# Optimization experiments

Measured on AMD Instinct MI355X. Metric: run time of the kernel, lower is better.

Reference implementation:

```python
import jax, jax.numpy as jnp
import numpy as np

H_DIM = 768
NUM_HEADS = 12
HEAD_DIM = H_DIM // NUM_HEADS
ROPE_BASE = 10000.0


def rope_cos_sin(seq_len, dim):
    inv_freq = 1.0 / (ROPE_BASE ** (jnp.arange(0, dim, 2, dtype=jnp.float32) / dim))
    t = jnp.arange(seq_len, dtype=jnp.float32)
    freqs = jnp.outer(t, inv_freq)              # [seq, dim/2]
    emb = jnp.concatenate([freqs, freqs], axis=-1)  # [seq, dim]
    return jnp.cos(emb), jnp.sin(emb)


def rotate_half(x):
    x1, x2 = jnp.split(x, 2, axis=-1)
    return jnp.concatenate([-x2, x1], axis=-1)


def setup_inputs() -> dict:
    key = jax.random.key(0)
    ks = jax.random.split(key, 9)
    s = 1.0 / np.sqrt(H_DIM)
    inp = {
        'x': jax.random.normal(ks[0], (2, 8, 1024, H_DIM), dtype=jnp.float32),
        'Wq': jax.random.normal(ks[1], (H_DIM, H_DIM), dtype=jnp.float32) * s,
        'bq': jnp.zeros((H_DIM,), dtype=jnp.float32),
        'Wk': jax.random.normal(ks[2], (H_DIM, H_DIM), dtype=jnp.float32) * s,
        'bk': jnp.zeros((H_DIM,), dtype=jnp.float32),
        'Wv': jax.random.normal(ks[3], (H_DIM, H_DIM), dtype=jnp.float32) * s,
        'bv': jnp.zeros((H_DIM,), dtype=jnp.float32),
        'Wo': jax.random.normal(ks[4], (H_DIM, H_DIM), dtype=jnp.float32) * s,
        'bo': jnp.zeros((H_DIM,), dtype=jnp.float32),
        'mask': jnp.ones((2, 8, 1, 1, 1024), dtype=jnp.int32),
    }
    return inp


def reference(x, Wq, bq, Wk, bk, Wv, bv, Wo, bo, mask):
    b, r, s, d = x.shape
    H, D = NUM_HEADS, HEAD_DIM

    def proj(W, bvec):
        # [b,r,s,d] -> [b,r,H,s,D]
        y = x @ W + bvec
        return y.reshape(b, r, s, H, D).transpose(0, 1, 3, 2, 4)

    q = proj(Wq, bq)
    k = proj(Wk, bk)
    v = proj(Wv, bv)

    cos, sin = rope_cos_sin(s, D)   # [s, D]
    cos = cos[None, None, None]     # broadcast over b,r,H
    sin = sin[None, None, None]
    q = q * cos + rotate_half(q) * sin
    k = k * cos + rotate_half(k) * sin

    scores = jnp.einsum('brhqd,brhkd->brhqk', q, k) / jnp.sqrt(jnp.float32(D))
    scores = jnp.where(mask == 0, -jnp.inf, scores)
    probs = jax.nn.softmax(scores, axis=-1)  # dropout is identity in eval
    out = jnp.einsum('brhqk,brhkd->brhqd', probs, v)
    out = out.transpose(0, 1, 3, 2, 4).reshape(b, r, s, d)
    return out @ Wo + bo
```

## Files before the change

kernel.cpp:

```cpp
#include <hip/hip_runtime.h>


#define M_TOT 16384
#define DM    768
#define NH    12
#define HD    64
#define SEQ   1024

typedef __attribute__((ext_vector_type(8))) __bf16 bf16x8;
typedef __attribute__((ext_vector_type(4))) __bf16 bf16x4;
typedef __attribute__((ext_vector_type(4))) short s16x4;
typedef __attribute__((ext_vector_type(4))) float  f32x4;

static __device__ __forceinline__ unsigned short f2b(float f) {
  unsigned u = __builtin_bit_cast(unsigned, f);
  u += 0x7FFFu + ((u >> 16) & 1u);
  return (unsigned short)(u >> 16);
}
static __device__ __forceinline__ float b2f(unsigned short s) {
  unsigned u = ((unsigned)s) << 16;
  return __builtin_bit_cast(float, u);
}
static __device__ __forceinline__ unsigned cvt_pk_bf16(float lo, float hi) {
  unsigned d;
  asm("v_cvt_pk_bf16_f32 %0, %1, %2" : "=v"(d) : "v"(lo), "v"(hi));
  return d;
}

static __device__ __forceinline__ f32x4 mfma16(uint2 a, uint2 b, f32x4 c) {
#if __has_builtin(__builtin_amdgcn_mfma_f32_16x16x16_bf16)
  union U { uint2 u; bf16x4 v; } A, B;
  A.u = a; B.u = b;
  return __builtin_amdgcn_mfma_f32_16x16x16_bf16(A.v, B.v, c, 0, 0, 0);
#else
  union U { uint2 u; s16x4 v; } A, B;
  A.u = a; B.u = b;
  return __builtin_amdgcn_mfma_f32_16x16x16bf16_1k(A.v, B.v, c, 0, 0, 0);
#endif
}

static __device__ __forceinline__ void gl_lds16(const void* g, void* l) {
  __builtin_amdgcn_global_load_lds(
      (const __attribute__((address_space(1))) unsigned*)g,
      (__attribute__((address_space(3))) unsigned*)l, 16, 0, 0);
}

static __device__ __forceinline__ int swz_src(int c) {
  return ((c >> 3) << 6) + (((c & 7) ^ ((c >> 3) & 7)) << 3);
}
static __device__ __forceinline__ int swz_rd(int row, int col16) {
  return (row << 6) + ((col16 ^ (row & 7)) << 3);
}

__global__ void cvt_x(const float* __restrict__ x, unsigned short* __restrict__ xb) {
  const int n4 = M_TOT * DM / 4;
  for (int i = blockIdx.x * blockDim.x + threadIdx.x; i < n4; i += gridDim.x * blockDim.x) {
    float4 v = ((const float4*)x)[i];
    ushort4 o;
    o.x = f2b(v.x); o.y = f2b(v.y); o.z = f2b(v.z); o.w = f2b(v.w);
    ((ushort4*)xb)[i] = o;
  }
}

__global__ void prep_w(const float* __restrict__ Wq, const float* __restrict__ Wk,
                       const float* __restrict__ Wv, const float* __restrict__ Wo,
                       unsigned short* __restrict__ Wt) {
  __shared__ float T[64][65];
  const int wsel = blockIdx.z;
  const float* W = wsel == 0 ? Wq : wsel == 1 ? Wk : wsel == 2 ? Wv : Wo;
  const int k0 = blockIdx.x * 64, n0 = blockIdx.y * 64;
  const int t = threadIdx.x;
#pragma unroll
  for (int p = 0; p < 16; ++p) {
    int e = p * 256 + t, r = e >> 6, c = e & 63;
    T[r][c] = W[(size_t)(k0 + r) * DM + n0 + c];
  }
  __syncthreads();
  unsigned short* dst = Wt + (size_t)wsel * DM * DM;
#pragma unroll
  for (int p = 0; p < 16; ++p) {
    int e = p * 256 + t, r = e >> 6, c = e & 63;
    dst[(size_t)(n0 + r) * DM + k0 + c] = f2b(T[c][r]);
  }
}

__global__ void rope_tab(float* __restrict__ cosT, float* __restrict__ sinT) {
  int i = blockIdx.x * blockDim.x + threadIdx.x;
  int s = i >> 5, j = i & 31;
  float inv = powf(10000.0f, -(float)j * (1.0f / 32.0f));
  float ang = (float)s * inv;
  cosT[i] = cosf(ang);
  sinT[i] = sinf(ang);
}

__global__ void bias_cat(const float* __restrict__ bq, const float* __restrict__ bk,
                         const float* __restrict__ bv, float* __restrict__ bcat) {
  int i = blockIdx.x * 256 + threadIdx.x;
  if (i < 3 * DM)
    bcat[i] = i < DM ? bq[i] : (i < 2 * DM ? bk[i - DM] : bv[i - 2 * DM]);
}

static __device__ __forceinline__ void gemm_core(const unsigned short* __restrict__ A,
                                                 const unsigned short* __restrict__ Bt,
                                                 int m0, int n0, f32x4 acc[4][4],
                                                 char* smem) {
  unsigned short* As = (unsigned short*)smem;
  unsigned short* Bs = As + 128 * 64;
  const int tid = threadIdx.x, lane = tid & 63, w = tid >> 6;
  const int wr = w >> 1, wc = w & 1;
  const int lr = lane & 15, g4 = lane >> 4;

#pragma unroll
  for (int i = 0; i < 4; ++i)
#pragma unroll
    for (int j = 0; j < 4; ++j) acc[i][j] = (f32x4){0.f, 0.f, 0.f, 0.f};

  for (int kt = 0; kt < DM / 64; ++kt) {
    const int k0 = kt * 64;
#pragma unroll
    for (int p = 0; p < 4; ++p) {
      int cb = p * 256 + w * 64;
      int c = cb + lane;
      gl_lds16(A + (size_t)(m0 + (c >> 3)) * DM + k0 + (c & 7) * 8, (char*)As + cb * 16);
      gl_lds16(Bt + (size_t)(n0 + (c >> 3)) * DM + k0 + (c & 7) * 8, (char*)Bs + cb * 16);
    }
    __syncthreads();
#pragma unroll
    for (int kk = 0; kk < 2; ++kk) {
      const int ko = kk * 32 + g4 * 8;
      bf16x8 a[4], b[4];
#pragma unroll
      for (int i = 0; i < 4; ++i) a[i] = *(const bf16x8*)&As[(wr * 64 + i * 16 + lr) * 64 + ko];
#pragma unroll
      for (int j = 0; j < 4; ++j) b[j] = *(const bf16x8*)&Bs[(wc * 64 + j * 16 + lr) * 64 + ko];
#pragma unroll
      for (int i = 0; i < 4; ++i)
#pragma unroll
        for (int j = 0; j < 4; ++j)
          acc[i][j] = __builtin_amdgcn_mfma_f32_16x16x32_bf16(a[i], b[j], acc[i][j], 0, 0, 0);
    }
    __syncthreads();
  }
}

__global__ __launch_bounds__(256, 4) void gemm_qkv(
    const unsigned short* __restrict__ xb, const unsigned short* __restrict__ Wt,
    const float* __restrict__ bcat, const float* __restrict__ cosT,
    const float* __restrict__ sinT, unsigned short* __restrict__ Qh,
    unsigned short* __restrict__ Kh, unsigned short* __restrict__ Vt) {
  __shared__ alignas(16) char smem[32768];
  const int m0 = blockIdx.x * 128, n0 = blockIdx.y * 128;
  f32x4 acc[4][4];
  gemm_core(xb, Wt, m0, n0, acc, smem);

  const int tid = threadIdx.x, lane = tid & 63, w = tid >> 6;
  const int wr = w >> 1, wc = w & 1;
  const int lr = lane & 15, g4 = lane >> 4;
  const int zone = blockIdx.y / 6;
  const int wcol0 = n0 - zone * DM + wc * 64;
  const int h = wcol0 >> 6;
  const int br = m0 >> 10;
  const int s_base = (m0 & 1023) + wr * 64;

  if (zone == 2) {
    unsigned short* dstb = Vt + ((size_t)(br * NH + h) * HD) * SEQ;
#pragma unroll
    for (int j = 0; j < 4; ++j) {
      const int d = j * 16 + lr;
      const float bv = bcat[n0 + wc * 64 + d];
#pragma unroll
      for (int i = 0; i < 4; ++i) {
        const int s0 = s_base + i * 16 + g4 * 4;
        ushort4 st;
        st.x = f2b(acc[i][j][0] + bv);
        st.y = f2b(acc[i][j][1] + bv);
        st.z = f2b(acc[i][j][2] + bv);
        st.w = f2b(acc[i][j][3] + bv);
        *(ushort4*)&dstb[(size_t)d * SEQ + s0] = st;
      }
    }
  } else {
    const float sc = zone == 0 ? 0.125f * 1.44269504f : 1.0f;
    unsigned short* dstb = (zone ? Kh : Qh) + ((size_t)(br * NH + h) * SEQ) * HD;
    char* Wb = smem + (size_t)w * 8192;
    const int s_q = s_base + lane;
    const int bcol = n0 + wc * 64;

#pragma unroll
    for (int hh = 0; hh < 2; ++hh) {
#pragma unroll
      for (int jj = 0; jj < 2; ++jj) {
        const int jp = hh + jj * 2;
        const float bv = bcat[bcol + jp * 16 + lr];
        const int dslot = jj * 16 + lr;
        const int sub = (dslot & 3) * 4;
        const int ch = dslot >> 2;
#pragma unroll
        for (int i = 0; i < 4; ++i) {
#pragma unroll
          for (int r = 0; r < 4; ++r) {
            const int s_loc = i * 16 + g4 * 4 + r;
            *(float*)(Wb + s_loc * 128 + ((ch ^ (s_loc & 7)) << 4) + sub) =
                (acc[i][jp][r] + bv) * sc;
          }
        }
      }
      unsigned short* drow = dstb + (size_t)s_q * HD + hh * 16;
      const char* Rb = Wb + lane * 128;
      const int lx = lane & 7;
#pragma unroll
      for (int c = 0; c < 4; ++c) {
        f32x4 va = *(const f32x4*)(Rb + ((c ^ lx) << 4));
        f32x4 vb = *(const f32x4*)(Rb + (((c + 4) ^ lx) << 4));
        float4 c4 = *(const float4*)&cosT[s_q * 32 + hh * 16 + c * 4];
        float4 s4 = *(const float4*)&sinT[s_q * 32 + hh * 16 + c * 4];
        uint2 oa, ob;
        oa.x = cvt_pk_bf16(va[0] * c4.x - vb[0] * s4.x, va[1] * c4.y - vb[1] * s4.y);
        oa.y = cvt_pk_bf16(va[2] * c4.z - vb[2] * s4.z, va[3] * c4.w - vb[3] * s4.w);
        ob.x = cvt_pk_bf16(vb[0] * c4.x + va[0] * s4.x, vb[1] * c4.y + va[1] * s4.y);
        ob.y = cvt_pk_bf16(vb[2] * c4.z + va[2] * s4.z, vb[3] * c4.w + va[3] * s4.w);
        *(uint2*)(drow + c * 4)      = oa;
        *(uint2*)(drow + 32 + c * 4) = ob;
      }
    }
  }
}

__global__ __launch_bounds__(256, 4) void gemm_o(const unsigned short* __restrict__ attnb,
                                                 const unsigned short* __restrict__ WtO,
                                                 const float* __restrict__ bo,
                                                 float* __restrict__ out) {
  __shared__ alignas(16) char smem[32768];
  const int m0 = blockIdx.x * 128, n0 = blockIdx.y * 128;
  f32x4 acc[4][4];
  gemm_core(attnb, WtO, m0, n0, acc, smem);
  const int tid = threadIdx.x, lane = tid & 63, w = tid >> 6;
  const int wr = w >> 1, wc = w & 1;
  const int lr = lane & 15, g4 = lane >> 4;
#pragma unroll
  for (int j = 0; j < 4; ++j) {
    const int col = n0 + wc * 64 + j * 16 + lr;
    const float bv = bo[col];
#pragma unroll
    for (int i = 0; i < 4; ++i) {
      const int rowb = m0 + wr * 64 + i * 16 + g4 * 4;
#pragma unroll
      for (int r = 0; r < 4; ++r)
        out[(size_t)(rowb + r) * DM + col] = acc[i][j][r] + bv;
    }
  }
}

__global__ __launch_bounds__(256) void attn_fwd(const unsigned short* __restrict__ Qh,
                                                const unsigned short* __restrict__ Kh,
                                                const unsigned short* __restrict__ Vt,
                                                const int* __restrict__ mask,
                                                unsigned short* __restrict__ attnb) {
  __shared__ unsigned short Ks[64 * 64];
  __shared__ unsigned short Vs[64 * 64];
  __shared__ float Msf[SEQ];
  const int qt = blockIdx.x, brh = blockIdx.y;
  const int br = brh / NH, h = brh - br * NH;
  const int tid = threadIdx.x, lane = tid & 63, w = tid >> 6;
  const int lr = lane & 15, g4 = lane >> 4;

  {
    int4 mi = *(const int4*)&mask[(size_t)br * SEQ + tid * 4];
    float4 mf;
    mf.x = mi.x ? 0.f : -3e38f;
    mf.y = mi.y ? 0.f : -3e38f;
    mf.z = mi.z ? 0.f : -3e38f;
    mf.w = mi.w ? 0.f : -3e38f;
    *(float4*)&Msf[tid * 4] = mf;
  }

  const unsigned short* Qg = Qh + ((size_t)brh * SEQ + qt * 64 + w * 16 + lr) * HD;
  bf16x8 qa[2];
  qa[0] = *(const bf16x8*)(Qg + g4 * 8);
  qa[1] = *(const bf16x8*)(Qg + 32 + g4 * 8);

  f32x4 o[4];
#pragma unroll
  for (int j = 0; j < 4; ++j) o[j] = (f32x4){0.f, 0.f, 0.f, 0.f};
  float m = -INFINITY;
  float lpA = 0.f, lpB = 0.f;

  const unsigned short* Kg = Kh + (size_t)brh * SEQ * HD;
  const unsigned short* Vg = Vt + (size_t)brh * HD * SEQ;

  for (int kb = 0; kb < SEQ / 64; ++kb) {
#pragma unroll
    for (int p = 0; p < 2; ++p) {
      int cb = p * 256 + w * 64;
      int c = cb + lane;
      gl_lds16(Kg + (size_t)kb * 64 * HD + swz_src(c), (char*)Ks + cb * 16);
      gl_lds16(Vg + (size_t)(c >> 3) * SEQ + kb * 64 + (((c & 7) ^ ((c >> 3) & 7)) << 3),
               (char*)Vs + cb * 16);
    }
    __syncthreads();

    f32x4 s4[4];
#pragma unroll
    for (int j = 0; j < 4; ++j) s4[j] = (f32x4){0.f, 0.f, 0.f, 0.f};
    __builtin_amdgcn_s_setprio(1);
#pragma unroll
    for (int kk = 0; kk < 2; ++kk) {
#pragma unroll
      for (int j = 0; j < 4; ++j) {
        bf16x8 kf = *(const bf16x8*)&Ks[swz_rd(j * 16 + lr, kk * 4 + g4)];
        s4[j] = __builtin_amdgcn_mfma_f32_16x16x32_bf16(kf, qa[kk], s4[j], 0, 0, 0);
      }
    }
    __builtin_amdgcn_s_setprio(0);

    float sv[4][4];
#pragma unroll
    for (int j = 0; j < 4; ++j) {
      float4 mq = *(const float4*)&Msf[kb * 64 + j * 16 + g4 * 4];
      sv[j][0] = s4[j][0] + mq.x;
      sv[j][1] = s4[j][1] + mq.y;
      sv[j][2] = s4[j][2] + mq.z;
      sv[j][3] = s4[j][3] + mq.w;
    }

    float mx = sv[0][0];
#pragma unroll
    for (int j = 0; j < 4; ++j)
#pragma unroll
      for (int r = 0; r < 4; ++r) mx = fmaxf(mx, sv[j][r]);
    mx = fmaxf(mx, __shfl_xor(mx, 16));
    mx = fmaxf(mx, __shfl_xor(mx, 32));
    if (!__all(mx <= m + 8.0f)) {
      float mnew = fmaxf(m, mx);
      float sc = exp2f(m - mnew);
      lpA *= sc; lpB *= sc;
#pragma unroll
      for (int j = 0; j < 4; ++j)
#pragma unroll
        for (int r = 0; r < 4; ++r) o[j][r] *= sc;
      m = mnew;
    }

    uint2 wb[4];
#pragma unroll
    for (int j = 0; j < 4; ++j) {
      float p0 = exp2f(sv[j][0] - m), p1 = exp2f(sv[j][1] - m);
      float p2 = exp2f(sv[j][2] - m), p3 = exp2f(sv[j][3] - m);
      if (j & 1) lpB += (p0 + p1) + (p2 + p3);
      else       lpA += (p0 + p1) + (p2 + p3);
      wb[j].x = cvt_pk_bf16(p0, p1);
      wb[j].y = cvt_pk_bf16(p2, p3);
    }

    __builtin_amdgcn_s_setprio(1);
#pragma unroll
    for (int jj = 0; jj < 4; ++jj) {
      const int row = jj * 16 + lr;
#pragma unroll
      for (int j = 0; j < 4; ++j) {
        const int c8 = j * 4 + g4;
        uint2 av = *(const uint2*)&Vs[(row << 6) + ((((c8 >> 1) ^ (lr & 7))) << 3) +
                                      ((c8 & 1) << 2)];
        o[jj] = mfma16(av, wb[j], o[jj]);
      }
    }
    __builtin_amdgcn_s_setprio(0);
    __syncthreads();
  }

  float lp = lpA + lpB;
  float l = lp + __shfl_xor(lp, 16);
  l += __shfl_xor(l, 32);
  float inv = l > 0.f ? 1.0f / l : 0.f;
  unsigned short* dst =
      attnb + ((size_t)(br * SEQ + qt * 64 + w * 16 + lr)) * DM + h * HD;
#pragma unroll
  for (int j = 0; j < 4; ++j) {
    ushort4 st;
    st.x = f2b(o[j][0] * inv);
    st.y = f2b(o[j][1] * inv);
    st.z = f2b(o[j][2] * inv);
    st.w = f2b(o[j][3] * inv);
    *(ushort4*)&dst[j * 16 + g4 * 4] = st;
  }
}

extern "C" void kernel_launch(void* const* d_in, const int* in_sizes, int n_in,
                              void* d_out, int out_size, void* d_ws, size_t ws_size,
                              hipStream_t stream) {
  const float* x  = (const float*)d_in[0];
  const float* Wq = (const float*)d_in[1];
  const float* bq = (const float*)d_in[2];
  const float* Wk = (const float*)d_in[3];
  const float* bk = (const float*)d_in[4];
  const float* Wv = (const float*)d_in[5];
  const float* bv = (const float*)d_in[6];
  const float* Wo = (const float*)d_in[7];
  const float* bo = (const float*)d_in[8];
  const int* mask = (const int*)d_in[9];
  float* out = (float*)d_out;

  const size_t OFF_XB   = 0;
  const size_t OFF_WT   = 25165824;
  const size_t OFF_COS  = 29884416;
  const size_t OFF_SIN  = 30015488;
  const size_t OFF_BC   = 30146560;
  const size_t OFF_ATT  = 30158848;
  const size_t OFF_QH   = 55324672;
  const size_t OFF_KH   = 80490496;
  const size_t OFF_VT   = 105656320;
  const size_t REQUIRED = 130822144;
  if (ws_size < REQUIRED) return;

  char* w = (char*)d_ws;
  unsigned short* xb   = (unsigned short*)(w + OFF_XB);
  unsigned short* Wt   = (unsigned short*)(w + OFF_WT);
  float* cosT          = (float*)(w + OFF_COS);
  float* sinT          = (float*)(w + OFF_SIN);
  float* bcat          = (float*)(w + OFF_BC);
  unsigned short* attnb = (unsigned short*)(w + OFF_ATT);
  unsigned short* Qh   = (unsigned short*)(w + OFF_QH);
  unsigned short* Kh   = (unsigned short*)(w + OFF_KH);
  unsigned short* Vt   = (unsigned short*)(w + OFF_VT);

  cvt_x<<<2048, 256, 0, stream>>>(x, xb);
  prep_w<<<dim3(12, 12, 4), 256, 0, stream>>>(Wq, Wk, Wv, Wo, Wt);
  rope_tab<<<128, 256, 0, stream>>>(cosT, sinT);
  bias_cat<<<9, 256, 0, stream>>>(bq, bk, bv, bcat);
  gemm_qkv<<<dim3(128, 18), 256, 0, stream>>>(xb, Wt, bcat, cosT, sinT, Qh, Kh, Vt);
  attn_fwd<<<dim3(16, 192), 256, 0, stream>>>(Qh, Kh, Vt, mask, attnb);
  gemm_o<<<dim3(128, 6), 256, 0, stream>>>(attnb, Wt + (size_t)3 * DM * DM, bo, out);
}
```

Before: 268.0 us.

## Double-buffer K/V tiles in attention and skip mask add when all keys live

The attention kernel now keeps two LDS buffers for K and V and issues the async global-to-LDS loads for the next key block before computing on the current one, dropping one barrier per iteration. It also checks once per block whether the whole mask row is nonzero and, if so, skips the per-tile mask loads and adds. The row max is computed with a three-input max tree. The cost is double the K/V LDS footprint, which may lower occupancy. The loop also relies on the end-of-iteration barrier to cover the in-flight async loads, so correctness depends on the compiler inserting a vmcnt wait before that barrier.

```diff
diff --git a/kernel.cpp b/kernel.cpp
--- a/kernel.cpp
+++ b/kernel.cpp
@@ -26,6 +26,7 @@
   asm("v_cvt_pk_bf16_f32 %0, %1, %2" : "=v"(d) : "v"(lo), "v"(hi));
   return d;
 }
+#define MAX3(a, b, c) fmaxf(fmaxf((a), (b)), (c))
 
 static __device__ __forceinline__ f32x4 mfma16(uint2 a, uint2 b, f32x4 c) {
 #if __has_builtin(__builtin_amdgcn_mfma_f32_16x16x16_bf16)
@@ -256,16 +257,20 @@
                                                 const unsigned short* __restrict__ Vt,
                                                 const int* __restrict__ mask,
                                                 unsigned short* __restrict__ attnb) {
-  __shared__ unsigned short Ks[64 * 64];
-  __shared__ unsigned short Vs[64 * 64];
+  __shared__ unsigned short Ks[2][64 * 64];
+  __shared__ unsigned short Vs[2][64 * 64];
   __shared__ float Msf[SEQ];
   const int qt = blockIdx.x, brh = blockIdx.y;
   const int br = brh / NH, h = brh - br * NH;
   const int tid = threadIdx.x, lane = tid & 63, w = tid >> 6;
   const int lr = lane & 15, g4 = lane >> 4;
 
-  {
-    int4 mi = *(const int4*)&mask[(size_t)br * SEQ + tid * 4];
+  const unsigned short* Kg = Kh + (size_t)brh * SEQ * HD;
+  const unsigned short* Vg = Vt + (size_t)brh * HD * SEQ;
+
+  int4 mi = *(const int4*)&mask[(size_t)br * SEQ + tid * 4];
+  const int allLive = __syncthreads_and(mi.x && mi.y && mi.z && mi.w);
+  if (!allLive) {
     float4 mf;
     mf.x = mi.x ? 0.f : -3e38f;
     mf.y = mi.y ? 0.f : -3e38f;
@@ -274,6 +279,15 @@
     *(float4*)&Msf[tid * 4] = mf;
   }
 
+#pragma unroll
+  for (int p = 0; p < 2; ++p) {
+    int cb = p * 256 + w * 64;
+    int c = cb + lane;
+    gl_lds16(Kg + swz_src(c), (char*)Ks[0] + cb * 16);
+    gl_lds16(Vg + (size_t)(c >> 3) * SEQ + (((c & 7) ^ ((c >> 3) & 7)) << 3),
+             (char*)Vs[0] + cb * 16);
+  }
+
   const unsigned short* Qg = Qh + ((size_t)brh * SEQ + qt * 64 + w * 16 + lr) * HD;
   bf16x8 qa[2];
   qa[0] = *(const bf16x8*)(Qg + g4 * 8);
@@ -285,19 +299,25 @@
   float m = -INFINITY;
   float lpA = 0.f, lpB = 0.f;
 
-  const unsigned short* Kg = Kh + (size_t)brh * SEQ * HD;
-  const unsigned short* Vg = Vt + (size_t)brh * HD * SEQ;
+  __syncthreads();
+
+  unsigned short* KsC = Ks[0];
+  unsigned short* VsC = Vs[0];
+  unsigned short* KsN = Ks[1];
+  unsigned short* VsN = Vs[1];
 
   for (int kb = 0; kb < SEQ / 64; ++kb) {
-#pragma unroll
-    for (int p = 0; p < 2; ++p) {
-      int cb = p * 256 + w * 64;
-      int c = cb + lane;
-      gl_lds16(Kg + (size_t)kb * 64 * HD + swz_src(c), (char*)Ks + cb * 16);
-      gl_lds16(Vg + (size_t)(c >> 3) * SEQ + kb * 64 + (((c & 7) ^ ((c >> 3) & 7)) << 3),
-               (char*)Vs + cb * 16);
-    }
-    __syncthreads();
+    if (kb + 1 < SEQ / 64) {
+#pragma unroll
+      for (int p = 0; p < 2; ++p) {
+        int cb = p * 256 + w * 64;
+        int c = cb + lane;
+        gl_lds16(Kg + (size_t)(kb + 1) * 64 * HD + swz_src(c), (char*)KsN + cb * 16);
+        gl_lds16(Vg + (size_t)(c >> 3) * SEQ + (kb + 1) * 64 +
+                     (((c & 7) ^ ((c >> 3) & 7)) << 3),
+                 (char*)VsN + cb * 16);
+      }
+    }
 
     f32x4 s4[4];
 #pragma unroll
@@ -307,27 +327,35 @@
     for (int kk = 0; kk < 2; ++kk) {
 #pragma unroll
       for (int j = 0; j < 4; ++j) {
-        bf16x8 kf = *(const bf16x8*)&Ks[swz_rd(j * 16 + lr, kk * 4 + g4)];
+        bf16x8 kf = *(const bf16x8*)&KsC[swz_rd(j * 16 + lr, kk * 4 + g4)];
         s4[j] = __builtin_amdgcn_mfma_f32_16x16x32_bf16(kf, qa[kk], s4[j], 0, 0, 0);
       }
     }
     __builtin_amdgcn_s_setprio(0);
 
     float sv[4][4];
-#pragma unroll
-    for (int j = 0; j < 4; ++j) {
-      float4 mq = *(const float4*)&Msf[kb * 64 + j * 16 + g4 * 4];
-      sv[j][0] = s4[j][0] + mq.x;
-      sv[j][1] = s4[j][1] + mq.y;
-      sv[j][2] = s4[j][2] + mq.z;
-      sv[j][3] = s4[j][3] + mq.w;
-    }
-
-    float mx = sv[0][0];
-#pragma unroll
-    for (int j = 0; j < 4; ++j)
-#pragma unroll
-      for (int r = 0; r < 4; ++r) mx = fmaxf(mx, sv[j][r]);
+    if (allLive) {
+#pragma unroll
+      for (int j = 0; j < 4; ++j)
+#pragma unroll
+        for (int r = 0; r < 4; ++r) sv[j][r] = s4[j][r];
+    } else {
+#pragma unroll
+      for (int j = 0; j < 4; ++j) {
+        float4 mq = *(const float4*)&Msf[kb * 64 + j * 16 + g4 * 4];
+        sv[j][0] = s4[j][0] + mq.x;
+        sv[j][1] = s4[j][1] + mq.y;
+        sv[j][2] = s4[j][2] + mq.z;
+        sv[j][3] = s4[j][3] + mq.w;
+      }
+    }
+
+    float t0 = MAX3(sv[0][0], sv[0][1], sv[0][2]);
+    float t1 = MAX3(sv[0][3], sv[1][0], sv[1][1]);
+    float t2 = MAX3(sv[1][2], sv[1][3], sv[2][0]);
+    float t3 = MAX3(sv[2][1], sv[2][2], sv[2][3]);
+    float t4 = MAX3(sv[3][0], sv[3][1], sv[3][2]);
+    float mx = fmaxf(MAX3(t0, t1, sv[3][3]), MAX3(t2, t3, t4));
     mx = fmaxf(mx, __shfl_xor(mx, 16));
     mx = fmaxf(mx, __shfl_xor(mx, 32));
     if (!__all(mx <= m + 8.0f)) {
@@ -359,13 +387,17 @@
 #pragma unroll
       for (int j = 0; j < 4; ++j) {
         const int c8 = j * 4 + g4;
-        uint2 av = *(const uint2*)&Vs[(row << 6) + ((((c8 >> 1) ^ (lr & 7))) << 3) +
-                                      ((c8 & 1) << 2)];
+        uint2 av = *(const uint2*)&VsC[(row << 6) + ((((c8 >> 1) ^ (lr & 7))) << 3) +
+                                       ((c8 & 1) << 2)];
         o[jj] = mfma16(av, wb[j], o[jj]);
       }
     }
     __builtin_amdgcn_s_setprio(0);
+
     __syncthreads();
+    unsigned short* t;
+    t = KsC; KsC = KsN; KsN = t;
+    t = VsC; VsC = VsN; VsN = t;
   }
 
   float lp = lpA + lpB;
```

Result: no change. 264.9 us (-1.2%).
